# Kernel tuning notes

Measured on AMD Instinct MI355X. Metric: run time of the kernel, lower is better.

The kernel has to match this reference:

```python
import jax, jax.numpy as jnp
import numpy as np

EMBED = 8192      # DYNAMIC(2048) + STATIC(6144)
U0, U1 = 1024, 256  # units
EGO = 3
NUM_HEAD = 6
ACTION = 2
MEAN_SCALE = 5.0
INIT_STD = 5.0
MIN_STD = 1e-4
BATCH = 8192


def setup_inputs() -> dict:
    key = jax.random.key(0)
    ks = jax.random.split(key, 10)
    s = lambda fan_in: 1.0 / np.sqrt(fan_in)
    x = jax.random.normal(ks[0], (BATCH, EMBED), dtype=jnp.float32)
    # command head index in [0, 6) == RoadOption.value - 1
    command = jax.random.randint(ks[1], (BATCH,), 0, NUM_HEAD, dtype=jnp.int32)
    ego_state = jax.random.normal(ks[2], (BATCH, EGO), dtype=jnp.float32)
    # shared trunk fc: Linear(EMBED -> U0)
    fc_W = jax.random.uniform(ks[3], (EMBED, U0), jnp.float32, -s(EMBED), s(EMBED))
    fc_b = jax.random.uniform(ks[4], (U0,), jnp.float32, -s(EMBED), s(EMBED))
    # per-head MLP: Linear(U0+EGO -> U1) -> ReLU -> Linear(U1 -> 2*ACTION)
    cin = U0 + EGO
    W1 = jax.random.uniform(ks[5], (NUM_HEAD, cin, U1), jnp.float32, -s(cin), s(cin))
    b1 = jax.random.uniform(ks[6], (NUM_HEAD, U1), jnp.float32, -s(cin), s(cin))
    W2 = jax.random.uniform(ks[7], (NUM_HEAD, U1, 2 * ACTION), jnp.float32, -s(U1), s(U1))
    b2 = jax.random.uniform(ks[8], (NUM_HEAD, 2 * ACTION), jnp.float32, -s(U1), s(U1))
    return {"x": x, "command": command, "ego_state": ego_state,
            "fc_W": fc_W, "fc_b": fc_b, "W1": W1, "b1": b1, "W2": W2, "b2": b2}


def reference(x, command, ego_state, fc_W, fc_b, W1, b1, W2, b2):
    # shared trunk: Linear + ReLU, then concat ego state -> [B, U0+EGO]
    h = jax.nn.relu(x @ fc_W + fc_b)
    h = jnp.concatenate([h, ego_state], axis=-1)
    # routed heads: compute all 6 small heads densely, then select per sample
    # (faithful math; an optimized kernel would gather->grouped GEMM->scatter)
    h1 = jax.nn.relu(jnp.einsum('bi,hio->bho', h, W1) + b1)          # [B, H, U1]
    h2 = jnp.einsum('bhi,hio->bho', h1, W2) + b2                      # [B, H, 2A]
    sel = jnp.take_along_axis(h2, command[:, None, None].astype(jnp.int32), axis=1)
    out = sel[:, 0, :]                                                # [B, 2A]
    mean, std = jnp.split(out, 2, axis=-1)
    mean = MEAN_SCALE * jnp.tanh(mean / MEAN_SCALE)
    raw_init_std = np.float32(np.log(np.exp(INIT_STD) - 1.0))
    std = jax.nn.softplus(std + raw_init_std) + MIN_STD
    # distribution parameters (pre TanhBijector Normal params)
    return jnp.concatenate([mean, std], axis=-1)
```

## Files before the change

kernel.cpp:

```cpp
#include <hip/hip_runtime.h>
#include <stdint.h>

typedef short bf16x8 __attribute__((ext_vector_type(8)));
typedef float f32x4 __attribute__((ext_vector_type(4)));

#define BATCH 8192
#define EMBED 8192
#define U0    1024
#define U1    256
#define NHEAD 6

__device__ __forceinline__ unsigned short f2bf(float f) {
  union { float f; unsigned int u; } v; v.f = f;
  unsigned int u = v.u;
  unsigned int r = u + 0x7FFFu + ((u >> 16) & 1u);
  return (unsigned short)(r >> 16);
}
__device__ __forceinline__ unsigned int pk2(float lo, float hi) {
  return (unsigned int)f2bf(lo) | ((unsigned int)f2bf(hi) << 16);
}
__device__ __forceinline__ void async_copy16(const void* g, void* l) {
  __builtin_amdgcn_global_load_lds((const __attribute__((address_space(1))) void*)g,
                                   (__attribute__((address_space(3))) void*)l, 16, 0, 0);
}

__global__ void cvt_x_kernel(const float* __restrict__ x, unsigned short* __restrict__ xb) {
  long i = ((long)blockIdx.x * 256 + threadIdx.x) * 8;
  float4 a = *(const float4*)(x + i);
  float4 b = *(const float4*)(x + i + 4);
  uint4 r;
  r.x = pk2(a.x, a.y); r.y = pk2(a.z, a.w);
  r.z = pk2(b.x, b.y); r.w = pk2(b.z, b.w);
  *(uint4*)(xb + i) = r;
}

__global__ void transpose_cvt_kernel(const float* __restrict__ in, unsigned short* __restrict__ out,
                                     int R, int C, long in_z, long out_z) {
  __shared__ unsigned short tile[64][65];
  const float* inp = in + (long)blockIdx.z * in_z;
  unsigned short* outp = out + (long)blockIdx.z * out_z;
  int r0 = blockIdx.x * 64;
  int c0 = blockIdx.y * 64;
  int lc = threadIdx.x & 63;
  int lr = threadIdx.x >> 6;
#pragma unroll
  for (int i = 0; i < 16; i++) {
    int r = lr + i * 4;
    tile[r][lc] = f2bf(inp[(long)(r0 + r) * C + (c0 + lc)]);
  }
  __syncthreads();
#pragma unroll
  for (int i = 0; i < 16; i++) {
    int c = lr + i * 4;
    outp[(long)(c0 + c) * R + (r0 + lc)] = tile[lc][c];
  }
}

__global__ void bucket_kernel(const int* __restrict__ cmd, int* __restrict__ idxlist,
                              int* __restrict__ meta) {
  __shared__ int cnt[NHEAD], cur[NHEAD], off[NHEAD + 1];
  int tid = threadIdx.x;
  int lane = tid & 63, wave = tid >> 6;
  if (tid < NHEAD) cnt[tid] = 0;
  __syncthreads();
  for (int base = wave * 64; base < BATCH; base += 1024) {
    int c = cmd[base + lane];
#pragma unroll
    for (int h2 = 0; h2 < NHEAD; h2++) {
      unsigned long long m = __ballot(c == h2);
      if (lane == 0 && m) atomicAdd(&cnt[h2], __popcll(m));
    }
  }
  __syncthreads();
  if (tid == 0) {
    int s = 0;
    for (int h2 = 0; h2 < NHEAD; h2++) { off[h2] = s; s += cnt[h2]; }
    off[NHEAD] = s;
  }
  __syncthreads();
  if (tid < NHEAD) cur[tid] = off[tid];
  if (tid <= NHEAD) meta[tid] = off[tid];
  __syncthreads();
  for (int base = wave * 64; base < BATCH; base += 1024) {
    int b = base + lane;
    int c = cmd[b];
    int pos = 0;
#pragma unroll
    for (int h2 = 0; h2 < NHEAD; h2++) {
      unsigned long long m = __ballot(c == h2);
      if (m) {
        int leader = (int)(__ffsll((unsigned long long)m) - 1);
        int wbase = 0;
        if (lane == leader) wbase = atomicAdd(&cur[h2], __popcll(m));
        wbase = __shfl(wbase, leader);
        if (c == h2) pos = wbase + __popcll(m & ((1ULL << lane) - 1ULL));
      }
    }
    idxlist[pos] = b;
  }
}

__global__ __launch_bounds__(512) void gemm_kernel(const unsigned short* __restrict__ xb,
                                                   const unsigned short* __restrict__ wt,
                                                   const float* __restrict__ fc_b,
                                                   unsigned short* __restrict__ h) {
  __shared__ uint4 As[1024];
  __shared__ uint4 Bs[1024];
  int tid  = threadIdx.x;
  int lane = tid & 63;
  int wave = tid >> 6;
  int wm = wave >> 1;
  int wn = wave & 1;

  int f = blockIdx.x;
  int xcd = f & 7;
  int idx = f >> 3;
  int by = xcd * 8 + (idx >> 3);
  int bx = idx & 7;
  int m0 = by * 128;
  int n0 = bx * 128;
  int l15 = lane & 15, lq = lane >> 4;

  long asrc[2], bsrc[2];
#pragma unroll
  for (int j = 0; j < 2; j++) {
    int ca = wave * 2 + j;
    int cwm = ca >> 2, cka = (ca >> 1) & 1, cmi = ca & 1;
    asrc[j] = (long)(m0 + cwm * 32 + cmi * 16 + l15) * EMBED + cka * 32 + lq * 8;
    int cb = wave * 2 + j;
    int cwn = cb >> 3, ckb = (cb >> 2) & 1, cni = cb & 3;
    bsrc[j] = (long)(n0 + cwn * 64 + cni * 16 + l15) * EMBED + ckb * 32 + lq * 8;
  }

  f32x4 zero = {0.f, 0.f, 0.f, 0.f};
  f32x4 acc[2][4];
#pragma unroll
  for (int mi = 0; mi < 2; mi++)
#pragma unroll
    for (int ni = 0; ni < 4; ni++) acc[mi][ni] = zero;

  for (int k0 = 0; k0 < EMBED; k0 += 64) {
    __syncthreads();
#pragma unroll
    for (int j = 0; j < 2; j++) {
      int c = wave * 2 + j;
      async_copy16(xb + asrc[j] + k0, &As[c * 64 + lane]);
      async_copy16(wt + bsrc[j] + k0, &Bs[c * 64 + lane]);
    }
    __syncthreads();
#pragma unroll
    for (int ks = 0; ks < 2; ks++) {
      bf16x8 af[2], bfr[4];
#pragma unroll
      for (int mi = 0; mi < 2; mi++) af[mi] = *(const bf16x8*)&As[((wm * 2 + ks) * 2 + mi) * 64 + lane];
#pragma unroll
      for (int ni = 0; ni < 4; ni++) bfr[ni] = *(const bf16x8*)&Bs[((wn * 2 + ks) * 4 + ni) * 64 + lane];
#pragma unroll
      for (int mi = 0; mi < 2; mi++)
#pragma unroll
        for (int ni = 0; ni < 4; ni++)
          acc[mi][ni] = __builtin_amdgcn_mfma_f32_16x16x32_bf16(af[mi], bfr[ni], acc[mi][ni], 0, 0, 0);
    }
  }

#pragma unroll
  for (int ni = 0; ni < 4; ni++) {
    int col = n0 + wn * 64 + ni * 16 + l15;
    float bias = fc_b[col];
#pragma unroll
    for (int mi = 0; mi < 2; mi++) {
      int rbase = m0 + wm * 32 + mi * 16 + lq * 4;
#pragma unroll
      for (int r = 0; r < 4; r++) {
        float v = acc[mi][ni][r] + bias;
        v = v > 0.f ? v : 0.f;
        h[(long)(rbase + r) * U0 + col] = f2bf(v);
      }
    }
  }
}

__global__ __launch_bounds__(256) void head_kernel(const unsigned short* __restrict__ h,
                                                   const unsigned short* __restrict__ w1t,
                                                   const float* __restrict__ W1,
                                                   const float* __restrict__ b1,
                                                   const float* __restrict__ W2,
                                                   const float* __restrict__ b2,
                                                   const float* __restrict__ ego,
                                                   const int* __restrict__ idxlist,
                                                   const int* __restrict__ meta,
                                                   float* __restrict__ out) {
  int hd = blockIdx.y;
  int off = meta[hd];
  int cnt = meta[hd + 1] - off;
  int t0 = blockIdx.x * 32;
  if (t0 >= cnt) return;

  __shared__ int ridx[32];
  __shared__ float h1s[32][257];
  __shared__ float w2s[1024];
  int tid = threadIdx.x;
  if (tid < 32) {
    int i = t0 + tid;
    ridx[tid] = idxlist[off + (i < cnt ? i : 0)];
  }
  *(float4*)&w2s[tid * 4] = *(const float4*)(W2 + (long)hd * 1024 + tid * 4);
  __syncthreads();

  int lane = tid & 63, wave = tid >> 6;
  int l15 = lane & 15, lq = lane >> 4;

  long abase[2];
#pragma unroll
  for (int mi = 0; mi < 2; mi++) abase[mi] = (long)ridx[mi * 16 + l15] * U0 + lq * 8;
  long bbase[4];
#pragma unroll
  for (int ni = 0; ni < 4; ni++)
    bbase[ni] = (long)(hd * 256 + wave * 64 + ni * 16 + l15) * 1024 + lq * 8;

  f32x4 zero = {0.f, 0.f, 0.f, 0.f};
  f32x4 acc[2][4];
#pragma unroll
  for (int mi = 0; mi < 2; mi++)
#pragma unroll
    for (int ni = 0; ni < 4; ni++) acc[mi][ni] = zero;

#pragma unroll 2
  for (int k0 = 0; k0 < 1024; k0 += 32) {
    bf16x8 af[2], bfr[4];
#pragma unroll
    for (int mi = 0; mi < 2; mi++) af[mi] = *(const bf16x8*)(h + abase[mi] + k0);
#pragma unroll
    for (int ni = 0; ni < 4; ni++) bfr[ni] = *(const bf16x8*)(w1t + bbase[ni] + k0);
#pragma unroll
    for (int mi = 0; mi < 2; mi++)
#pragma unroll
      for (int ni = 0; ni < 4; ni++)
        acc[mi][ni] = __builtin_amdgcn_mfma_f32_16x16x32_bf16(af[mi], bfr[ni], acc[mi][ni], 0, 0, 0);
  }

  const float* W1e = W1 + (long)hd * 1027 * 256 + (long)1024 * 256;
#pragma unroll
  for (int mi = 0; mi < 2; mi++)
#pragma unroll
    for (int r = 0; r < 4; r++) {
      int rl = mi * 16 + lq * 4 + r;
      int b = ridx[rl];
      float e0 = ego[b * 3 + 0], e1 = ego[b * 3 + 1], e2 = ego[b * 3 + 2];
#pragma unroll
      for (int ni = 0; ni < 4; ni++) {
        int col = wave * 64 + ni * 16 + l15;
        float v = acc[mi][ni][r] + b1[hd * 256 + col]
                + e0 * W1e[col] + e1 * W1e[256 + col] + e2 * W1e[512 + col];
        h1s[rl][col] = v > 0.f ? v : 0.f;
      }
    }
  __syncthreads();

  if (tid < 128) {
    int t = tid >> 2, o2 = tid & 3;
    if (t0 + t < cnt) {
      float s0 = 0.f, s1 = 0.f, s2 = 0.f, s3 = 0.f;
#pragma unroll 4
      for (int i = 0; i < 256; i += 4) {
        s0 += h1s[t][i + 0] * w2s[(i + 0) * 4 + o2];
        s1 += h1s[t][i + 1] * w2s[(i + 1) * 4 + o2];
        s2 += h1s[t][i + 2] * w2s[(i + 2) * 4 + o2];
        s3 += h1s[t][i + 3] * w2s[(i + 3) * 4 + o2];
      }
      float sum = b2[hd * 4 + o2] + ((s0 + s1) + (s2 + s3));
      int b = ridx[t];
      float res;
      if (o2 < 2) {
        res = 5.0f * tanhf(sum * 0.2f);
      } else {
        float z = sum + 4.99323838f;
        res = (z > 20.f ? z : log1pf(expf(z))) + 1e-4f;
      }
      out[b * 4 + o2] = res;
    }
  }
}

extern "C" void kernel_launch(void* const* d_in, const int* in_sizes, int n_in,
                              void* d_out, int out_size, void* d_ws, size_t ws_size,
                              hipStream_t stream) {
  const float* x   = (const float*)d_in[0];
  const int*   cmd = (const int*)d_in[1];
  const float* ego = (const float*)d_in[2];
  const float* fcW = (const float*)d_in[3];
  const float* fcb = (const float*)d_in[4];
  const float* W1  = (const float*)d_in[5];
  const float* b1  = (const float*)d_in[6];
  const float* W2  = (const float*)d_in[7];
  const float* b2  = (const float*)d_in[8];
  float* out = (float*)d_out;

  char* ws = (char*)d_ws;
  unsigned short* xb   = (unsigned short*)(ws);
  unsigned short* wt   = (unsigned short*)(ws + 134217728);
  unsigned short* hbuf = (unsigned short*)(ws + 150994944);
  unsigned short* w1t  = (unsigned short*)(ws + 167772160);
  int* idxlist         = (int*)(ws + 170917888);
  int* meta            = (int*)(ws + 170950656);

  hipLaunchKernelGGL(cvt_x_kernel, dim3(32768), dim3(256), 0, stream, x, xb);
  hipLaunchKernelGGL(transpose_cvt_kernel, dim3(128, 16, 1), dim3(256), 0, stream,
                     fcW, wt, 8192, 1024, 0L, 0L);
  hipLaunchKernelGGL(transpose_cvt_kernel, dim3(16, 4, 6), dim3(256), 0, stream,
                     W1, w1t, 1024, 256, (long)1027 * 256, (long)256 * 1024);
  hipLaunchKernelGGL(bucket_kernel, dim3(1), dim3(1024), 0, stream, cmd, idxlist, meta);
  hipLaunchKernelGGL(gemm_kernel, dim3(512), dim3(512), 0, stream, xb, wt, fcb, hbuf);
  hipLaunchKernelGGL(head_kernel, dim3(256, 6), dim3(256), 0, stream,
                     hbuf, w1t, W1, b1, W2, b2, ego, idxlist, meta, out);
}
```

Baseline: 755.3 us.

## Split trunk GEMM over K into two halves with a separate reduce kernel

The trunk GEMM now splits the 8192-long K dimension into two halves. Each block computes a full 128x128 tile with 4 waves and 4x4 MFMA fragments per wave, and writes bf16 partial sums to a doubled workspace. A new reduce kernel adds the two partials, applies bias and ReLU, and writes h in place. The x conversion kernel also becomes a grid-stride loop over fewer blocks. This doubles the GEMM's block count, at the cost of an extra pass over the partial buffer and bf16 rounding of the partial sums before they are added.

```diff
diff --git a/kernel.cpp b/kernel.cpp
--- a/kernel.cpp
+++ b/kernel.cpp
@@ -25,13 +25,16 @@
 }
 
 __global__ void cvt_x_kernel(const float* __restrict__ x, unsigned short* __restrict__ xb) {
-  long i = ((long)blockIdx.x * 256 + threadIdx.x) * 8;
-  float4 a = *(const float4*)(x + i);
-  float4 b = *(const float4*)(x + i + 4);
-  uint4 r;
-  r.x = pk2(a.x, a.y); r.y = pk2(a.z, a.w);
-  r.z = pk2(b.x, b.y); r.w = pk2(b.z, b.w);
-  *(uint4*)(xb + i) = r;
+  const long total = (long)BATCH * EMBED;
+  const long stride = (long)gridDim.x * blockDim.x * 8;
+  for (long i = ((long)blockIdx.x * blockDim.x + threadIdx.x) * 8; i < total; i += stride) {
+    float4 a = *(const float4*)(x + i);
+    float4 b = *(const float4*)(x + i + 4);
+    uint4 r;
+    r.x = pk2(a.x, a.y); r.y = pk2(a.z, a.w);
+    r.z = pk2(b.x, b.y); r.w = pk2(b.z, b.w);
+    *(uint4*)(xb + i) = r;
+  }
 }
 
 __global__ void transpose_cvt_kernel(const float* __restrict__ in, unsigned short* __restrict__ out,
@@ -100,84 +103,110 @@
   }
 }
 
-__global__ __launch_bounds__(512) void gemm_kernel(const unsigned short* __restrict__ xb,
+__global__ __launch_bounds__(256) void gemm_kernel(const unsigned short* __restrict__ xb,
                                                    const unsigned short* __restrict__ wt,
-                                                   const float* __restrict__ fc_b,
-                                                   unsigned short* __restrict__ h) {
+                                                   unsigned short* __restrict__ pbuf) {
   __shared__ uint4 As[1024];
   __shared__ uint4 Bs[1024];
   int tid  = threadIdx.x;
   int lane = tid & 63;
   int wave = tid >> 6;
-  int wm = wave >> 1;
-  int wn = wave & 1;
+  int wm = wave >> 1, wn = wave & 1;
 
   int f = blockIdx.x;
   int xcd = f & 7;
-  int idx = f >> 3;
-  int by = xcd * 8 + (idx >> 3);
-  int bx = idx & 7;
+  int g = f >> 3;
+  int by = xcd * 8 + (g >> 4);
+  int rem = g & 15;
+  int kh = rem >> 3;
+  int bx = rem & 7;
   int m0 = by * 128;
   int n0 = bx * 128;
   int l15 = lane & 15, lq = lane >> 4;
 
-  long asrc[2], bsrc[2];
-#pragma unroll
-  for (int j = 0; j < 2; j++) {
-    int ca = wave * 2 + j;
-    int cwm = ca >> 2, cka = (ca >> 1) & 1, cmi = ca & 1;
-    asrc[j] = (long)(m0 + cwm * 32 + cmi * 16 + l15) * EMBED + cka * 32 + lq * 8;
-    int cb = wave * 2 + j;
-    int cwn = cb >> 3, ckb = (cb >> 2) & 1, cni = cb & 3;
-    bsrc[j] = (long)(n0 + cwn * 64 + cni * 16 + l15) * EMBED + ckb * 32 + lq * 8;
+  long asrc[4], bsrc[4];
+#pragma unroll
+  for (int j = 0; j < 4; j++) {
+    int c = wave * 4 + j;
+    int cwm = c >> 3, cks = (c >> 2) & 1, cmi = c & 3;
+    int kofs = cks * 32 + lq * 8;
+    asrc[j] = (long)(m0 + cwm * 64 + cmi * 16 + l15) * EMBED + kofs;
+    bsrc[j] = (long)(n0 + cwm * 64 + cmi * 16 + l15) * EMBED + kofs;
   }
 
   f32x4 zero = {0.f, 0.f, 0.f, 0.f};
-  f32x4 acc[2][4];
-#pragma unroll
-  for (int mi = 0; mi < 2; mi++)
+  f32x4 acc[4][4];
+#pragma unroll
+  for (int mi = 0; mi < 4; mi++)
 #pragma unroll
     for (int ni = 0; ni < 4; ni++) acc[mi][ni] = zero;
 
-  for (int k0 = 0; k0 < EMBED; k0 += 64) {
+  const int kbeg = kh * 4096;
+  for (int k0 = kbeg; k0 < kbeg + 4096; k0 += 64) {
     __syncthreads();
 #pragma unroll
-    for (int j = 0; j < 2; j++) {
-      int c = wave * 2 + j;
+    for (int j = 0; j < 4; j++) {
+      int c = wave * 4 + j;
       async_copy16(xb + asrc[j] + k0, &As[c * 64 + lane]);
       async_copy16(wt + bsrc[j] + k0, &Bs[c * 64 + lane]);
     }
     __syncthreads();
 #pragma unroll
     for (int ks = 0; ks < 2; ks++) {
-      bf16x8 af[2], bfr[4];
-#pragma unroll
-      for (int mi = 0; mi < 2; mi++) af[mi] = *(const bf16x8*)&As[((wm * 2 + ks) * 2 + mi) * 64 + lane];
+      bf16x8 af[4], bfr[4];
+#pragma unroll
+      for (int mi = 0; mi < 4; mi++) af[mi] = *(const bf16x8*)&As[((wm * 2 + ks) * 4 + mi) * 64 + lane];
 #pragma unroll
       for (int ni = 0; ni < 4; ni++) bfr[ni] = *(const bf16x8*)&Bs[((wn * 2 + ks) * 4 + ni) * 64 + lane];
 #pragma unroll
-      for (int mi = 0; mi < 2; mi++)
+      for (int mi = 0; mi < 4; mi++)
 #pragma unroll
         for (int ni = 0; ni < 4; ni++)
           acc[mi][ni] = __builtin_amdgcn_mfma_f32_16x16x32_bf16(af[mi], bfr[ni], acc[mi][ni], 0, 0, 0);
     }
   }
 
+  unsigned short* p = pbuf + (long)kh * (8192L * 1024);
 #pragma unroll
   for (int ni = 0; ni < 4; ni++) {
     int col = n0 + wn * 64 + ni * 16 + l15;
-    float bias = fc_b[col];
-#pragma unroll
-    for (int mi = 0; mi < 2; mi++) {
-      int rbase = m0 + wm * 32 + mi * 16 + lq * 4;
+#pragma unroll
+    for (int mi = 0; mi < 4; mi++) {
+      int rbase = m0 + wm * 64 + mi * 16 + lq * 4;
 #pragma unroll
       for (int r = 0; r < 4; r++) {
-        float v = acc[mi][ni][r] + bias;
-        v = v > 0.f ? v : 0.f;
-        h[(long)(rbase + r) * U0 + col] = f2bf(v);
-      }
-    }
-  }
+        p[(long)(rbase + r) * U0 + col] = f2bf(acc[mi][ni][r]);
+      }
+    }
+  }
+}
+
+__global__ __launch_bounds__(256) void reduce_kernel(unsigned short* __restrict__ pb,
+                                                     const float* __restrict__ fc_b) {
+  long i = ((long)blockIdx.x * 256 + threadIdx.x) * 8;
+  const unsigned short* p1 = pb + 8192L * 1024;
+  uint4 a = *(const uint4*)(pb + i);
+  uint4 b = *(const uint4*)(p1 + i);
+  int cb = (int)(i & (U0 - 1));
+  float4 b0 = *(const float4*)(fc_b + cb);
+  float4 b1 = *(const float4*)(fc_b + cb + 4);
+  const unsigned int* aw = (const unsigned int*)&a;
+  const unsigned int* bw = (const unsigned int*)&b;
+  float bias[8] = {b0.x, b0.y, b0.z, b0.w, b1.x, b1.y, b1.z, b1.w};
+  uint4 r;
+  unsigned int* rw = (unsigned int*)&r;
+#pragma unroll
+  for (int j = 0; j < 4; j++) {
+    union { unsigned int u; float f; } lo0, hi0, lo1, hi1;
+    lo0.u = (aw[j] & 0xFFFFu) << 16; hi0.u = aw[j] & 0xFFFF0000u;
+    lo1.u = (bw[j] & 0xFFFFu) << 16; hi1.u = bw[j] & 0xFFFF0000u;
+    float vlo = lo0.f + lo1.f + bias[2 * j];
+    float vhi = hi0.f + hi1.f + bias[2 * j + 1];
+    vlo = vlo > 0.f ? vlo : 0.f;
+    vhi = vhi > 0.f ? vhi : 0.f;
+    rw[j] = pk2(vlo, vhi);
+  }
+  *(uint4*)(pb + i) = r;
 }
 
 __global__ __launch_bounds__(256) void head_kernel(const unsigned short* __restrict__ h,
@@ -299,18 +328,20 @@
   char* ws = (char*)d_ws;
   unsigned short* xb   = (unsigned short*)(ws);
   unsigned short* wt   = (unsigned short*)(ws + 134217728);
-  unsigned short* hbuf = (unsigned short*)(ws + 150994944);
-  unsigned short* w1t  = (unsigned short*)(ws + 167772160);
-  int* idxlist         = (int*)(ws + 170917888);
-  int* meta            = (int*)(ws + 170950656);
-
-  hipLaunchKernelGGL(cvt_x_kernel, dim3(32768), dim3(256), 0, stream, x, xb);
+  unsigned short* pbuf = (unsigned short*)(ws + 150994944);
+  unsigned short* hbuf = pbuf;
+  unsigned short* w1t  = (unsigned short*)(ws + 184549376);
+  int* idxlist         = (int*)(ws + 187695104);
+  int* meta            = (int*)(ws + 187727872);
+
+  hipLaunchKernelGGL(cvt_x_kernel, dim3(2048), dim3(256), 0, stream, x, xb);
   hipLaunchKernelGGL(transpose_cvt_kernel, dim3(128, 16, 1), dim3(256), 0, stream,
                      fcW, wt, 8192, 1024, 0L, 0L);
   hipLaunchKernelGGL(transpose_cvt_kernel, dim3(16, 4, 6), dim3(256), 0, stream,
                      W1, w1t, 1024, 256, (long)1027 * 256, (long)256 * 1024);
   hipLaunchKernelGGL(bucket_kernel, dim3(1), dim3(1024), 0, stream, cmd, idxlist, meta);
-  hipLaunchKernelGGL(gemm_kernel, dim3(512), dim3(512), 0, stream, xb, wt, fcb, hbuf);
+  hipLaunchKernelGGL(gemm_kernel, dim3(1024), dim3(256), 0, stream, xb, wt, pbuf);
+  hipLaunchKernelGGL(reduce_kernel, dim3(4096), dim3(256), 0, stream, pbuf, fcb);
   hipLaunchKernelGGL(head_kernel, dim3(256, 6), dim3(256), 0, stream,
                      hbuf, w1t, W1, b1, W2, b2, ego, idxlist, meta, out);
 }
```

After: 828.8 us. 9.7% more time.

## Double-buffer trunk GEMM LDS tiles and grid-stride the x conversion

Applied to the files above, without the earlier changes.

The trunk GEMM now keeps two LDS buffers per operand and issues the async global-to-LDS loads for the next K tile before computing on the current one. This overlaps memory latency with MFMA work and cuts the loop from two barriers per iteration to one. Shared memory per block doubles, which may reduce occupancy. The x conversion kernel also switches to a grid-stride loop with far fewer blocks, to reduce block launch overhead.

```diff
diff --git a/kernel.cpp b/kernel.cpp
--- a/kernel.cpp
+++ b/kernel.cpp
@@ -25,13 +25,16 @@
 }
 
 __global__ void cvt_x_kernel(const float* __restrict__ x, unsigned short* __restrict__ xb) {
-  long i = ((long)blockIdx.x * 256 + threadIdx.x) * 8;
-  float4 a = *(const float4*)(x + i);
-  float4 b = *(const float4*)(x + i + 4);
-  uint4 r;
-  r.x = pk2(a.x, a.y); r.y = pk2(a.z, a.w);
-  r.z = pk2(b.x, b.y); r.w = pk2(b.z, b.w);
-  *(uint4*)(xb + i) = r;
+  const long total = (long)BATCH * EMBED;
+  const long stride = (long)gridDim.x * blockDim.x * 8;
+  for (long i = ((long)blockIdx.x * blockDim.x + threadIdx.x) * 8; i < total; i += stride) {
+    float4 a = *(const float4*)(x + i);
+    float4 b = *(const float4*)(x + i + 4);
+    uint4 r;
+    r.x = pk2(a.x, a.y); r.y = pk2(a.z, a.w);
+    r.z = pk2(b.x, b.y); r.w = pk2(b.z, b.w);
+    *(uint4*)(xb + i) = r;
+  }
 }
 
 __global__ void transpose_cvt_kernel(const float* __restrict__ in, unsigned short* __restrict__ out,
@@ -104,8 +107,8 @@
                                                    const unsigned short* __restrict__ wt,
                                                    const float* __restrict__ fc_b,
                                                    unsigned short* __restrict__ h) {
-  __shared__ uint4 As[1024];
-  __shared__ uint4 Bs[1024];
+  __shared__ uint4 As[2][1024];
+  __shared__ uint4 Bs[2][1024];
   int tid  = threadIdx.x;
   int lane = tid & 63;
   int wave = tid >> 6;
@@ -122,14 +125,17 @@
   int l15 = lane & 15, lq = lane >> 4;
 
   long asrc[2], bsrc[2];
+  int aslot[2], bslot[2];
 #pragma unroll
   for (int j = 0; j < 2; j++) {
     int ca = wave * 2 + j;
     int cwm = ca >> 2, cka = (ca >> 1) & 1, cmi = ca & 1;
     asrc[j] = (long)(m0 + cwm * 32 + cmi * 16 + l15) * EMBED + cka * 32 + lq * 8;
+    aslot[j] = ca * 64 + lane;
     int cb = wave * 2 + j;
     int cwn = cb >> 3, ckb = (cb >> 2) & 1, cni = cb & 3;
     bsrc[j] = (long)(n0 + cwn * 64 + cni * 16 + l15) * EMBED + ckb * 32 + lq * 8;
+    bslot[j] = cb * 64 + lane;
   }
 
   f32x4 zero = {0.f, 0.f, 0.f, 0.f};
@@ -139,28 +145,38 @@
 #pragma unroll
     for (int ni = 0; ni < 4; ni++) acc[mi][ni] = zero;
 
-  for (int k0 = 0; k0 < EMBED; k0 += 64) {
-    __syncthreads();
-#pragma unroll
-    for (int j = 0; j < 2; j++) {
-      int c = wave * 2 + j;
-      async_copy16(xb + asrc[j] + k0, &As[c * 64 + lane]);
-      async_copy16(wt + bsrc[j] + k0, &Bs[c * 64 + lane]);
-    }
-    __syncthreads();
+#pragma unroll
+  for (int j = 0; j < 2; j++) {
+    async_copy16(xb + asrc[j], &As[0][aslot[j]]);
+    async_copy16(wt + bsrc[j], &Bs[0][bslot[j]]);
+  }
+  __syncthreads();
+
+  int cur = 0;
+  for (int t = 0; t < 128; ++t) {
+    if (t < 127) {
+      long kn = (long)(t + 1) * 64;
+#pragma unroll
+      for (int j = 0; j < 2; j++) {
+        async_copy16(xb + asrc[j] + kn, &As[cur ^ 1][aslot[j]]);
+        async_copy16(wt + bsrc[j] + kn, &Bs[cur ^ 1][bslot[j]]);
+      }
+    }
 #pragma unroll
     for (int ks = 0; ks < 2; ks++) {
       bf16x8 af[2], bfr[4];
 #pragma unroll
-      for (int mi = 0; mi < 2; mi++) af[mi] = *(const bf16x8*)&As[((wm * 2 + ks) * 2 + mi) * 64 + lane];
-#pragma unroll
-      for (int ni = 0; ni < 4; ni++) bfr[ni] = *(const bf16x8*)&Bs[((wn * 2 + ks) * 4 + ni) * 64 + lane];
+      for (int mi = 0; mi < 2; mi++) af[mi] = *(const bf16x8*)&As[cur][((wm * 2 + ks) * 2 + mi) * 64 + lane];
+#pragma unroll
+      for (int ni = 0; ni < 4; ni++) bfr[ni] = *(const bf16x8*)&Bs[cur][((wn * 2 + ks) * 4 + ni) * 64 + lane];
 #pragma unroll
       for (int mi = 0; mi < 2; mi++)
 #pragma unroll
         for (int ni = 0; ni < 4; ni++)
           acc[mi][ni] = __builtin_amdgcn_mfma_f32_16x16x32_bf16(af[mi], bfr[ni], acc[mi][ni], 0, 0, 0);
     }
+    __syncthreads();
+    cur ^= 1;
   }
 
 #pragma unroll
@@ -304,7 +320,7 @@
   int* idxlist         = (int*)(ws + 170917888);
   int* meta            = (int*)(ws + 170950656);
 
-  hipLaunchKernelGGL(cvt_x_kernel, dim3(32768), dim3(256), 0, stream, x, xb);
+  hipLaunchKernelGGL(cvt_x_kernel, dim3(2048), dim3(256), 0, stream, x, xb);
   hipLaunchKernelGGL(transpose_cvt_kernel, dim3(128, 16, 1), dim3(256), 0, stream,
                      fcW, wt, 8192, 1024, 0L, 0L);
   hipLaunchKernelGGL(transpose_cvt_kernel, dim3(16, 4, 6), dim3(256), 0, stream,
```

After: 761.5 us. Within noise of the previous version (+0.8%).
